# Optimization experiments

Measured on AMD Instinct MI355X. Metric: run time of the kernel, lower is better.

The kernel has to match this reference:

```python
import jax, jax.numpy as jnp
import numpy as np

D = 1024  # model_dim; d_ff == model_dim in this module
EPS = 1e-6

def setup_inputs() -> dict:
    key = jax.random.key(0)
    ks = jax.random.split(key, 8)
    s = 1.0 / np.sqrt(D)
    sg = 1.0 / np.sqrt(2 * D)
    return {
        "x": jax.random.normal(ks[0], (8, 2048, D), dtype=jnp.float32),
        "w1": jax.random.uniform(ks[1], (D, D), jnp.float32, -s, s),
        "b1": jnp.zeros((D,), jnp.float32),
        "w2": jax.random.uniform(ks[2], (D, D), jnp.float32, -s, s),
        "b2": jnp.zeros((D,), jnp.float32),
        "ln_g": jnp.ones((D,), jnp.float32),
        "ln_b": jnp.zeros((D,), jnp.float32),
        "wg": jax.random.uniform(ks[3], (2 * D, 2 * D), jnp.float32, -sg, sg),
        "bg": jnp.zeros((2 * D,), jnp.float32),
    }

def _layernorm(x, g, b):
    mu = jnp.mean(x, axis=-1, keepdims=True)
    var = jnp.mean(jnp.square(x - mu), axis=-1, keepdims=True)
    return (x - mu) * jax.lax.rsqrt(var + EPS) * g + b

def reference(x, w1, b1, w2, b2, ln_g, ln_b, wg, bg):
    B, S, d = x.shape
    # cumulative average: tril-normalized mask matmul == prefix-sum / position
    denom = jnp.arange(1, S + 1, dtype=x.dtype)[:, None]  # [S,1]
    avg = jnp.cumsum(x, axis=1) / denom                    # [B,S,D]
    # PositionwiseFeedForward (dropout is identity at inference)
    inter = jax.nn.relu(_layernorm(avg, ln_g, ln_b) @ w1 + b1)
    avg_out = inter @ w2 + b2 + avg
    # gating
    gates = jnp.concatenate([x, avg_out], axis=-1) @ wg + bg  # [B,S,2D]
    in_g, fg_g = jnp.split(gates, 2, axis=-1)
    gated = jax.nn.sigmoid(in_g) * x + jax.nn.sigmoid(fg_g) * avg_out
    return gated, avg_out
```

## Files before the change

### kernel.cpp

```cpp
#include <hip/hip_runtime.h>

typedef unsigned short u16;
typedef __attribute__((ext_vector_type(8))) short short8;
typedef __attribute__((ext_vector_type(8))) unsigned short ushort8;
typedef __attribute__((ext_vector_type(4))) float f32x4;
typedef __attribute__((ext_vector_type(4))) unsigned short u16x4;

#define DEV static __device__ __forceinline__

DEV u16 f2bf(float f){
    unsigned u = __float_as_uint(f);
    u += 0x7fffu + ((u >> 16) & 1u);
    return (u16)(u >> 16);
}
DEV float bf2f(u16 h){ return __uint_as_float(((unsigned)h) << 16); }
DEV float sigm(float v){ return 1.f / (1.f + __expf(-v)); }

DEV f32x4 MF(short8 a, short8 b, f32x4 c){
    return __builtin_amdgcn_mfma_f32_16x16x32_bf16(a, b, c, 0, 0, 0);
}
DEV void gload16(const void* g, u16* l){
    __builtin_amdgcn_global_load_lds(
        (const __attribute__((address_space(1))) void*)g,
        (__attribute__((address_space(3))) void*)l, 16, 0, 0);
}
DEV void stage_half(const char* gp, size_t K2, u16* dst){
    gload16(gp, dst);
    gload16(gp + (K2 << 3), dst + 512);
}

#define SBAR()   asm volatile("s_barrier" ::: "memory")
#define WVM(n)   asm volatile("s_waitcnt vmcnt(" #n ")" ::: "memory")
#define WLG0()   asm volatile("s_waitcnt lgkmcnt(0)" ::: "memory")

constexpr int Bn = 8, Sn = 2048, Dn = 1024;
constexpr int CH = 128, NC = Sn / CH;
constexpr size_t NTOK = (size_t)Bn * Sn;

__global__ __launch_bounds__(256) void k_wcvt(const float* __restrict__ w,
                                              u16* __restrict__ wt,
                                              int Kd, int Nd)
{
    __shared__ float tile[32][33];
    int nbn = Nd / 32;
    int bk = blockIdx.x / nbn, bn = blockIdx.x % nbn;
    int lx = threadIdx.x & 31, ly = threadIdx.x >> 5;
    #pragma unroll
    for (int i = 0; i < 32; i += 8)
        tile[ly + i][lx] = w[(size_t)(bk * 32 + ly + i) * Nd + bn * 32 + lx];
    __syncthreads();
    #pragma unroll
    for (int i = 0; i < 32; i += 8)
        wt[(size_t)(bn * 32 + ly + i) * Kd + bk * 32 + lx] = f2bf(tile[lx][ly + i]);
}

__global__ __launch_bounds__(256) void k_psum(const float* __restrict__ x,
                                              float* __restrict__ part)
{
    int bx = blockIdx.x;
    int dblk = bx & 3; bx >>= 2;
    int c = bx & (NC - 1), b = bx >> 4;
    int d = dblk * 256 + threadIdx.x;
    const float* px = x + ((size_t)b * Sn + (size_t)c * CH) * Dn + d;
    float s = 0.f;
    #pragma unroll 4
    for (int i = 0; i < CH; i++) s += px[(size_t)i * Dn];
    part[((size_t)b * NC + c) * Dn + d] = s;
}

__global__ __launch_bounds__(256) void k_pscan(float* part)
{
    int g = blockIdx.x * 256 + threadIdx.x;
    int b = g >> 10, d = g & 1023;
    float run = 0.f;
    #pragma unroll
    for (int c = 0; c < NC; c++){
        size_t idx = ((size_t)b * NC + c) * Dn + d;
        float v = part[idx]; part[idx] = run; run += v;
    }
}

__global__ __launch_bounds__(256) void k_avg(const float* __restrict__ x,
                                             const float* __restrict__ part,
                                             float* __restrict__ avg,
                                             u16* __restrict__ cat)
{
    int bx = blockIdx.x;
    int dblk = bx & 3; bx >>= 2;
    int c = bx & (NC - 1), b = bx >> 4;
    int d = dblk * 256 + threadIdx.x;
    const float* px = x   + ((size_t)b * Sn + (size_t)c * CH) * Dn + d;
    float*       pa = avg + ((size_t)b * Sn + (size_t)c * CH) * Dn + d;
    u16*         pc = cat + ((size_t)b * Sn + (size_t)c * CH) * 2048 + d;
    float run = part[((size_t)b * NC + c) * Dn + d];
    for (int i = 0; i < CH; i++){
        float v = px[(size_t)i * Dn];
        run += v;
        int s = c * CH + i;
        pa[(size_t)i * Dn] = run / (float)(s + 1);
        pc[(size_t)i * 2048] = f2bf(v);
    }
}

__global__ __launch_bounds__(256) void k_ln(const float* __restrict__ avg,
                                            const float* __restrict__ g,
                                            const float* __restrict__ bta,
                                            u16* __restrict__ out)
{
    size_t row = blockIdx.x;
    int t = threadIdx.x;
    const float4* pr = (const float4*)(avg + row * Dn);
    float4 v = pr[t];
    float s = v.x + v.y + v.z + v.w;
    float q = v.x * v.x + v.y * v.y + v.z * v.z + v.w * v.w;
    #pragma unroll
    for (int o = 32; o > 0; o >>= 1){
        s += __shfl_down(s, o, 64);
        q += __shfl_down(q, o, 64);
    }
    __shared__ float rs[4], rq[4];
    __shared__ float smu, srstd;
    int wid = t >> 6, lane = t & 63;
    if (lane == 0){ rs[wid] = s; rq[wid] = q; }
    __syncthreads();
    if (t == 0){
        float S = rs[0] + rs[1] + rs[2] + rs[3];
        float Q = rq[0] + rq[1] + rq[2] + rq[3];
        float mu = S * (1.f / Dn);
        float var = Q * (1.f / Dn) - mu * mu;
        smu = mu; srstd = rsqrtf(var + 1e-6f);
    }
    __syncthreads();
    float mu = smu, rstd = srstd;
    int d0 = t * 4;
    float4 gg = ((const float4*)g)[t];
    float4 bb = ((const float4*)bta)[t];
    u16x4 o;
    o[0] = f2bf((v.x - mu) * rstd * gg.x + bb.x);
    o[1] = f2bf((v.y - mu) * rstd * gg.y + bb.y);
    o[2] = f2bf((v.z - mu) * rstd * gg.z + bb.z);
    o[3] = f2bf((v.w - mu) * rstd * gg.w + bb.w);
    *(u16x4*)(out + row * Dn + d0) = o;
}

template<int EPI>
__global__ __launch_bounds__(512, 2)
void k_gemm(const u16* __restrict__ A, const u16* __restrict__ Bt,
            const float* __restrict__ bias,
            float* __restrict__ of, u16* __restrict__ ob,
            const float* __restrict__ resid,
            const float* __restrict__ xg, const float* __restrict__ ag,
            int M, int N, int K)
{
    __shared__ u16 smem[2][2][2][8192];

    int nbn = (EPI == 3) ? 8 : (N >> 8);
    int nwg = (M >> 8) * nbn;
    int bid = blockIdx.x;
    int swz = (bid & 7) * (nwg >> 3) + (bid >> 3);
    int bm = swz / nbn, bn = swz - bm * nbn;
    int m0 = bm << 8;
    int n0 = (EPI == 3) ? (bn << 7) : (bn << 8);

    int tid  = threadIdx.x;
    int wid  = tid >> 6, lane = tid & 63;
    int wm   = wid >> 2, wn = wid & 3;
    int fr   = lane & 15, q = lane >> 4;

    int srow = (wid << 4) + (lane >> 3);
    int cb   = ((lane & 7) << 4) ^ (((lane >> 3) & 7) << 4);
    size_t K2 = (size_t)K * 2;
    int b1base = (EPI == 3) ? (1024 + n0) : (n0 + 128);
    const char* gA0 = (const char*)A  + (size_t)(m0 + srow) * K2 + cb;
    const char* gA1 = (const char*)A  + (size_t)(m0 + 128 + srow) * K2 + cb;
    const char* gB0 = (const char*)Bt + (size_t)(n0 + srow) * K2 + cb;
    const char* gB1 = (const char*)Bt + (size_t)(b1base + srow) * K2 + cb;
    int w16 = wid << 10;

    int xorE = (lane & 7) << 3;
    int cbE0 = ((q << 3) ^ xorE);
    int cbE1 = cbE0 ^ 32;
    int aOff = (wm * 64 + fr) * 64;
    int bOff = (wn * 32 + fr) * 64;

    f32x4 acc[8][4] = {};
    int NT = K >> 6;

    stage_half(gA0, K2, &smem[0][0][0][w16]);
    stage_half(gB0, K2, &smem[0][1][0][w16]);
    stage_half(gB1, K2, &smem[0][1][1][w16]);
    stage_half(gA1, K2, &smem[0][0][1][w16]);

    for (int kt = 0; kt < NT; kt++){
        int cur = kt & 1, nxt = cur ^ 1;
        bool pre = (kt + 1) < NT;
        size_t toff = (size_t)(kt + 1) * 128;
        const u16* cA = &smem[cur][0][0][0];
        const u16* cB = &smem[cur][1][0][0];

        short8 a0f[4][2], a1f[4][2], b0f[2][2], b1f[2][2];

        WVM(4); SBAR();
        #pragma unroll
        for (int mi = 0; mi < 4; mi++){
            a0f[mi][0] = *(const short8*)&cA[aOff + mi * 1024 + cbE0];
            a0f[mi][1] = *(const short8*)&cA[aOff + mi * 1024 + cbE1];
        }
        #pragma unroll
        for (int ni = 0; ni < 2; ni++){
            b0f[ni][0] = *(const short8*)&cB[bOff + ni * 1024 + cbE0];
            b0f[ni][1] = *(const short8*)&cB[bOff + ni * 1024 + cbE1];
        }
        if (pre) stage_half(gA0 + toff, K2, &smem[nxt][0][0][w16]);
        WLG0();
        __builtin_amdgcn_sched_barrier(0);
        __builtin_amdgcn_s_setprio(1);
        #pragma unroll
        for (int mi = 0; mi < 4; mi++)
            #pragma unroll
            for (int ni = 0; ni < 2; ni++){
                acc[mi][ni] = MF(a0f[mi][0], b0f[ni][0], acc[mi][ni]);
                acc[mi][ni] = MF(a0f[mi][1], b0f[ni][1], acc[mi][ni]);
            }
        __builtin_amdgcn_s_setprio(0);

        if (pre){ WVM(4); } else { WVM(2); }
        SBAR();
        #pragma unroll
        for (int ni = 0; ni < 2; ni++){
            b1f[ni][0] = *(const short8*)&cB[8192 + bOff + ni * 1024 + cbE0];
            b1f[ni][1] = *(const short8*)&cB[8192 + bOff + ni * 1024 + cbE1];
        }
        if (pre) stage_half(gB0 + toff, K2, &smem[nxt][1][0][w16]);
        WLG0();
        __builtin_amdgcn_sched_barrier(0);
        __builtin_amdgcn_s_setprio(1);
        #pragma unroll
        for (int mi = 0; mi < 4; mi++)
            #pragma unroll
            for (int ni = 0; ni < 2; ni++){
                acc[mi][ni + 2] = MF(a0f[mi][0], b1f[ni][0], acc[mi][ni + 2]);
                acc[mi][ni + 2] = MF(a0f[mi][1], b1f[ni][1], acc[mi][ni + 2]);
            }
        __builtin_amdgcn_s_setprio(0);

        if (pre){ WVM(4); } else { WVM(0); }
        SBAR();
        #pragma unroll
        for (int mi = 0; mi < 4; mi++){
            a1f[mi][0] = *(const short8*)&cA[8192 + aOff + mi * 1024 + cbE0];
            a1f[mi][1] = *(const short8*)&cA[8192 + aOff + mi * 1024 + cbE1];
        }
        if (pre) stage_half(gB1 + toff, K2, &smem[nxt][1][1][w16]);
        WLG0();
        __builtin_amdgcn_sched_barrier(0);
        __builtin_amdgcn_s_setprio(1);
        #pragma unroll
        for (int mi = 0; mi < 4; mi++)
            #pragma unroll
            for (int ni = 0; ni < 2; ni++){
                acc[mi + 4][ni + 2] = MF(a1f[mi][0], b1f[ni][0], acc[mi + 4][ni + 2]);
                acc[mi + 4][ni + 2] = MF(a1f[mi][1], b1f[ni][1], acc[mi + 4][ni + 2]);
            }
        __builtin_amdgcn_s_setprio(0);

        if (pre) stage_half(gA1 + toff, K2, &smem[nxt][0][1][w16]);
        __builtin_amdgcn_s_setprio(1);
        #pragma unroll
        for (int mi = 0; mi < 4; mi++)
            #pragma unroll
            for (int ni = 0; ni < 2; ni++){
                acc[mi + 4][ni] = MF(a1f[mi][0], b0f[ni][0], acc[mi + 4][ni]);
                acc[mi + 4][ni] = MF(a1f[mi][1], b0f[ni][1], acc[mi + 4][ni]);
            }
        __builtin_amdgcn_s_setprio(0);
    }

    int col = lane & 15, rb = q * 4;

    if constexpr (EPI == 3){
        u16* s_in = &smem[0][0][0][0];
        u16* s_fg = s_in + 32768;
        float bi[2], bf_[2];
        #pragma unroll
        for (int ni = 0; ni < 2; ni++){
            bi[ni]  = bias[n0 + wn * 32 + ni * 16 + col];
            bf_[ni] = bias[1024 + n0 + wn * 32 + ni * 16 + col];
        }
        SBAR();
        #pragma unroll
        for (int mi = 0; mi < 8; mi++){
            int lrow = ((mi & 4) << 5) + wm * 64 + ((mi & 3) << 4) + rb;
            #pragma unroll
            for (int ni = 0; ni < 2; ni++){
                int c  = wn * 32 + ni * 16 + col;
                int cp = c ^ (q << 4);
                #pragma unroll
                for (int r = 0; r < 4; r++){
                    int row = lrow + r;
                    s_in[row * 128 + cp] = f2bf(sigm(acc[mi][ni][r] + bi[ni]));
                    s_fg[row * 128 + cp] = f2bf(sigm(acc[mi][ni + 2][r] + bf_[ni]));
                }
            }
        }
        WLG0(); SBAR();
        int rbase = wid * 32;
        #pragma unroll
        for (int rg = 0; rg < 8; rg++){
            int b4  = rbase + rg * 4;
            int row = b4 + (lane >> 4);
            int sw  = ((b4 >> 2) & 3) << 4;
            int c0  = (lane & 15) * 8;
            int cp  = c0 ^ sw;
            ushort8 iv = *(const ushort8*)&s_in[row * 128 + cp];
            ushort8 fv = *(const ushort8*)&s_fg[row * 128 + cp];
            size_t gb = (size_t)(m0 + row) * Dn + n0 + c0;
            float4 x0 = *(const float4*)&xg[gb], x1 = *(const float4*)&xg[gb + 4];
            float4 a0 = *(const float4*)&ag[gb], a1 = *(const float4*)&ag[gb + 4];
            float4 o0, o1;
            o0.x = bf2f(iv[0]) * x0.x + bf2f(fv[0]) * a0.x;
            o0.y = bf2f(iv[1]) * x0.y + bf2f(fv[1]) * a0.y;
            o0.z = bf2f(iv[2]) * x0.z + bf2f(fv[2]) * a0.z;
            o0.w = bf2f(iv[3]) * x0.w + bf2f(fv[3]) * a0.w;
            o1.x = bf2f(iv[4]) * x1.x + bf2f(fv[4]) * a1.x;
            o1.y = bf2f(iv[5]) * x1.y + bf2f(fv[5]) * a1.y;
            o1.z = bf2f(iv[6]) * x1.z + bf2f(fv[6]) * a1.z;
            o1.w = bf2f(iv[7]) * x1.w + bf2f(fv[7]) * a1.w;
            *(float4*)&of[gb] = o0;
            *(float4*)&of[gb + 4] = o1;
        }
        return;
    }

    #pragma unroll
    for (int mi = 0; mi < 8; mi++){
        int lrow = m0 + ((mi & 4) << 5) + wm * 64 + ((mi & 3) << 4) + rb;
        #pragma unroll
        for (int ni = 0; ni < 4; ni++){
            int gn = n0 + ((ni & 2) << 6) + wn * 32 + ((ni & 1) << 4) + col;
            float bv = bias[gn];
            #pragma unroll
            for (int r = 0; r < 4; r++){
                int gm = lrow + r;
                float v = acc[mi][ni][r] + bv;
                if constexpr (EPI == 1){
                    ob[(size_t)gm * N + gn] = f2bf(fmaxf(v, 0.f));
                } else {
                    v += resid[(size_t)gm * N + gn];
                    of[(size_t)gm * N + gn] = v;
                    ob[(size_t)gm * 2 * N + N + gn] = f2bf(v);
                }
            }
        }
    }
}

extern "C" void kernel_launch(void* const* d_in, const int* in_sizes, int n_in,
                              void* d_out, int out_size, void* d_ws, size_t ws_size,
                              hipStream_t stream)
{
    const float* x   = (const float*)d_in[0];
    const float* w1  = (const float*)d_in[1];
    const float* b1  = (const float*)d_in[2];
    const float* w2  = (const float*)d_in[3];
    const float* b2  = (const float*)d_in[4];
    const float* lng = (const float*)d_in[5];
    const float* lnb = (const float*)d_in[6];
    const float* wg  = (const float*)d_in[7];
    const float* bg  = (const float*)d_in[8];

    float* gated   = (float*)d_out;
    float* avg_out = (float*)d_out + NTOK * Dn;

    char* ws = (char*)d_ws;
    u16*   w1t   = (u16*)  (ws + (0ull   << 20));
    u16*   w2t   = (u16*)  (ws + (2ull   << 20));
    u16*   wgt   = (u16*)  (ws + (4ull   << 20));
    float* part  = (float*)(ws + (12ull  << 20));
    float* avg   = (float*)(ws + (16ull  << 20));
    u16*   ln    = (u16*)  (ws + (80ull  << 20));
    u16*   inter = (u16*)  (ws + (112ull << 20));
    u16*   cat   = (u16*)  (ws + (144ull << 20));

    k_wcvt<<<dim3(32 * 32), 256, 0, stream>>>(w1, w1t, Dn, Dn);
    k_wcvt<<<dim3(32 * 32), 256, 0, stream>>>(w2, w2t, Dn, Dn);
    k_wcvt<<<dim3(64 * 64), 256, 0, stream>>>(wg, wgt, 2 * Dn, 2 * Dn);

    k_psum <<<dim3(Bn * NC * 4), 256, 0, stream>>>(x, part);
    k_pscan<<<dim3(Bn * Dn / 256), 256, 0, stream>>>(part);
    k_avg  <<<dim3(Bn * NC * 4), 256, 0, stream>>>(x, part, avg, cat);

    k_ln<<<dim3((int)NTOK), 256, 0, stream>>>(avg, lng, lnb, ln);

    k_gemm<1><<<dim3((int)(NTOK / 256) * (Dn / 256)), 512, 0, stream>>>(
        ln, w1t, b1, nullptr, inter, nullptr, nullptr, nullptr,
        (int)NTOK, Dn, Dn);
    k_gemm<2><<<dim3((int)(NTOK / 256) * (Dn / 256)), 512, 0, stream>>>(
        inter, w2t, b2, avg_out, cat, avg, nullptr, nullptr,
        (int)NTOK, Dn, Dn);

    k_gemm<3><<<dim3((int)(NTOK / 256) * 8), 512, 0, stream>>>(
        cat, wgt, bg, gated, nullptr, nullptr, x, avg_out,
        (int)NTOK, 2 * Dn, 2 * Dn);
}
```

Measured before the change: 338.5 us.

## Store avg in bf16, reuse bf16 cat in gating epilogue, deepen GEMM prefetch pipeline

The cumulative average is now stored as bf16 instead of fp32, which halves its write and read traffic in the layernorm and GEMM2 residual steps. The gating epilogue reads bf16 x and avg_out from the cat buffer already in memory, replacing the fp32 reads of x and avg_out. The GEMM main loop is rewritten into a software pipeline that keeps two k-tiles in flight, with finer-grained vmcnt/lgkmcnt waits and sched barriers. This costs accuracy: avg enters the residual and layernorm in bf16, and gating multiplies by bf16-rounded x and avg_out.

```diff
diff --git a/kernel.cpp b/kernel.cpp
--- a/kernel.cpp
+++ b/kernel.cpp
@@ -31,7 +31,8 @@
 
 #define SBAR()   asm volatile("s_barrier" ::: "memory")
 #define WVM(n)   asm volatile("s_waitcnt vmcnt(" #n ")" ::: "memory")
-#define WLG0()   asm volatile("s_waitcnt lgkmcnt(0)" ::: "memory")
+#define WLG(n)   asm volatile("s_waitcnt lgkmcnt(" #n ")" ::: "memory")
+#define SCB()    __builtin_amdgcn_sched_barrier(0)
 
 constexpr int Bn = 8, Sn = 2048, Dn = 1024;
 constexpr int CH = 128, NC = Sn / CH;
@@ -82,7 +83,7 @@
 
 __global__ __launch_bounds__(256) void k_avg(const float* __restrict__ x,
                                              const float* __restrict__ part,
-                                             float* __restrict__ avg,
+                                             u16* __restrict__ avg,
                                              u16* __restrict__ cat)
 {
     int bx = blockIdx.x;
@@ -90,27 +91,27 @@
     int c = bx & (NC - 1), b = bx >> 4;
     int d = dblk * 256 + threadIdx.x;
     const float* px = x   + ((size_t)b * Sn + (size_t)c * CH) * Dn + d;
-    float*       pa = avg + ((size_t)b * Sn + (size_t)c * CH) * Dn + d;
+    u16*         pa = avg + ((size_t)b * Sn + (size_t)c * CH) * Dn + d;
     u16*         pc = cat + ((size_t)b * Sn + (size_t)c * CH) * 2048 + d;
     float run = part[((size_t)b * NC + c) * Dn + d];
     for (int i = 0; i < CH; i++){
         float v = px[(size_t)i * Dn];
         run += v;
         int s = c * CH + i;
-        pa[(size_t)i * Dn] = run / (float)(s + 1);
+        pa[(size_t)i * Dn] = f2bf(run / (float)(s + 1));
         pc[(size_t)i * 2048] = f2bf(v);
     }
 }
 
-__global__ __launch_bounds__(256) void k_ln(const float* __restrict__ avg,
+__global__ __launch_bounds__(256) void k_ln(const u16* __restrict__ avg,
                                             const float* __restrict__ g,
                                             const float* __restrict__ bta,
                                             u16* __restrict__ out)
 {
     size_t row = blockIdx.x;
     int t = threadIdx.x;
-    const float4* pr = (const float4*)(avg + row * Dn);
-    float4 v = pr[t];
+    u16x4 hv = ((const u16x4*)(avg + row * Dn))[t];
+    float4 v = { bf2f(hv[0]), bf2f(hv[1]), bf2f(hv[2]), bf2f(hv[3]) };
     float s = v.x + v.y + v.z + v.w;
     float q = v.x * v.x + v.y * v.y + v.z * v.z + v.w * v.w;
     #pragma unroll
@@ -148,8 +149,7 @@
 void k_gemm(const u16* __restrict__ A, const u16* __restrict__ Bt,
             const float* __restrict__ bias,
             float* __restrict__ of, u16* __restrict__ ob,
-            const float* __restrict__ resid,
-            const float* __restrict__ xg, const float* __restrict__ ag,
+            const u16* __restrict__ resid,
             int M, int N, int K)
 {
     __shared__ u16 smem[2][2][2][8192];
@@ -184,96 +184,91 @@
     int bOff = (wn * 32 + fr) * 64;
 
     f32x4 acc[8][4] = {};
+    short8 a0f[4][2], a1f[4][2], b0f[2][2], b1f[2][2];
     int NT = K >> 6;
 
-    stage_half(gA0, K2, &smem[0][0][0][w16]);
-    stage_half(gB0, K2, &smem[0][1][0][w16]);
-    stage_half(gB1, K2, &smem[0][1][1][w16]);
-    stage_half(gA1, K2, &smem[0][0][1][w16]);
-
-    for (int kt = 0; kt < NT; kt++){
-        int cur = kt & 1, nxt = cur ^ 1;
-        bool pre = (kt + 1) < NT;
-        size_t toff = (size_t)(kt + 1) * 128;
-        const u16* cA = &smem[cur][0][0][0];
-        const u16* cB = &smem[cur][1][0][0];
-
-        short8 a0f[4][2], a1f[4][2], b0f[2][2], b1f[2][2];
-
-        WVM(4); SBAR();
-        #pragma unroll
-        for (int mi = 0; mi < 4; mi++){
-            a0f[mi][0] = *(const short8*)&cA[aOff + mi * 1024 + cbE0];
-            a0f[mi][1] = *(const short8*)&cA[aOff + mi * 1024 + cbE1];
-        }
-        #pragma unroll
-        for (int ni = 0; ni < 2; ni++){
-            b0f[ni][0] = *(const short8*)&cB[bOff + ni * 1024 + cbE0];
-            b0f[ni][1] = *(const short8*)&cB[bOff + ni * 1024 + cbE1];
-        }
-        if (pre) stage_half(gA0 + toff, K2, &smem[nxt][0][0][w16]);
-        WLG0();
-        __builtin_amdgcn_sched_barrier(0);
-        __builtin_amdgcn_s_setprio(1);
-        #pragma unroll
-        for (int mi = 0; mi < 4; mi++)
-            #pragma unroll
-            for (int ni = 0; ni < 2; ni++){
-                acc[mi][ni] = MF(a0f[mi][0], b0f[ni][0], acc[mi][ni]);
-                acc[mi][ni] = MF(a0f[mi][1], b0f[ni][1], acc[mi][ni]);
-            }
-        __builtin_amdgcn_s_setprio(0);
-
-        if (pre){ WVM(4); } else { WVM(2); }
+#define ST_A0(t) stage_half(gA0 + (size_t)(t) * 128, K2, &smem[(t)&1][0][0][w16])
+#define ST_A1(t) stage_half(gA1 + (size_t)(t) * 128, K2, &smem[(t)&1][0][1][w16])
+#define ST_B0(t) stage_half(gB0 + (size_t)(t) * 128, K2, &smem[(t)&1][1][0][w16])
+#define ST_B1(t) stage_half(gB1 + (size_t)(t) * 128, K2, &smem[(t)&1][1][1][w16])
+#define RD_A(Fr, t, half) { const u16* _p = &smem[(t)&1][0][half][0];           \
+    _Pragma("unroll") for (int i = 0; i < 4; i++){                              \
+        Fr[i][0] = *(const short8*)&_p[aOff + i * 1024 + cbE0];                 \
+        Fr[i][1] = *(const short8*)&_p[aOff + i * 1024 + cbE1]; } }
+#define RD_B(Fr, t, half) { const u16* _p = &smem[(t)&1][1][half][0];           \
+    _Pragma("unroll") for (int i = 0; i < 2; i++){                              \
+        Fr[i][0] = *(const short8*)&_p[bOff + i * 1024 + cbE0];                 \
+        Fr[i][1] = *(const short8*)&_p[bOff + i * 1024 + cbE1]; } }
+#define MMQ(Af, Bf, mo, no)                                                     \
+    __builtin_amdgcn_s_setprio(1);                                              \
+    _Pragma("unroll") for (int mi = 0; mi < 4; mi++)                            \
+        _Pragma("unroll") for (int ni = 0; ni < 2; ni++){                       \
+            acc[mi+(mo)][ni+(no)] = MF(Af[mi][0], Bf[ni][0], acc[mi+(mo)][ni+(no)]); \
+            acc[mi+(mo)][ni+(no)] = MF(Af[mi][1], Bf[ni][1], acc[mi+(mo)][ni+(no)]); \
+        }                                                                        \
+    __builtin_amdgcn_s_setprio(0);
+
+    ST_A0(0); ST_B0(0); ST_B1(0); ST_A1(0); ST_A0(1); ST_B0(1); ST_B1(1);
+    WVM(12); SBAR();
+    RD_A(a0f, 0, 0);
+
+    for (int t = 0; t + 2 < NT; ++t){
+        WVM(8); SBAR();
+        ST_A1(t + 1);
+        RD_B(b0f, t, 0); SCB();
+        RD_B(b1f, t, 1);
+        WLG(4); SCB();
+        MMQ(a0f, b0f, 0, 0);
+        WVM(8); SBAR();
+        ST_A0(t + 2);
+        RD_A(a1f, t, 1);
+        WLG(8); SCB();
+        MMQ(a0f, b1f, 0, 2);
         SBAR();
-        #pragma unroll
-        for (int ni = 0; ni < 2; ni++){
-            b1f[ni][0] = *(const short8*)&cB[8192 + bOff + ni * 1024 + cbE0];
-            b1f[ni][1] = *(const short8*)&cB[8192 + bOff + ni * 1024 + cbE1];
-        }
-        if (pre) stage_half(gB0 + toff, K2, &smem[nxt][1][0][w16]);
-        WLG0();
-        __builtin_amdgcn_sched_barrier(0);
-        __builtin_amdgcn_s_setprio(1);
-        #pragma unroll
-        for (int mi = 0; mi < 4; mi++)
-            #pragma unroll
-            for (int ni = 0; ni < 2; ni++){
-                acc[mi][ni + 2] = MF(a0f[mi][0], b1f[ni][0], acc[mi][ni + 2]);
-                acc[mi][ni + 2] = MF(a0f[mi][1], b1f[ni][1], acc[mi][ni + 2]);
-            }
-        __builtin_amdgcn_s_setprio(0);
-
-        if (pre){ WVM(4); } else { WVM(0); }
+        ST_B0(t + 2);
+        WLG(0); SCB();
+        MMQ(a1f, b1f, 4, 2);
+        WVM(10); SBAR();
+        ST_B1(t + 2);
+        RD_A(a0f, t + 1, 0);
+        WLG(8); SCB();
+        MMQ(a1f, b0f, 4, 0);
+    }
+    {
+        int t = NT - 2;
+        WVM(8); SBAR();
+        ST_A1(t + 1);
+        RD_B(b0f, t, 0); SCB();
+        RD_B(b1f, t, 1);
+        WLG(4); SCB();
+        MMQ(a0f, b0f, 0, 0);
+        WVM(8); SBAR();
+        RD_A(a1f, t, 1);
+        WLG(8); SCB();
+        MMQ(a0f, b1f, 0, 2);
         SBAR();
-        #pragma unroll
-        for (int mi = 0; mi < 4; mi++){
-            a1f[mi][0] = *(const short8*)&cA[8192 + aOff + mi * 1024 + cbE0];
-            a1f[mi][1] = *(const short8*)&cA[8192 + aOff + mi * 1024 + cbE1];
-        }
-        if (pre) stage_half(gB1 + toff, K2, &smem[nxt][1][1][w16]);
-        WLG0();
-        __builtin_amdgcn_sched_barrier(0);
-        __builtin_amdgcn_s_setprio(1);
-        #pragma unroll
-        for (int mi = 0; mi < 4; mi++)
-            #pragma unroll
-            for (int ni = 0; ni < 2; ni++){
-                acc[mi + 4][ni + 2] = MF(a1f[mi][0], b1f[ni][0], acc[mi + 4][ni + 2]);
-                acc[mi + 4][ni + 2] = MF(a1f[mi][1], b1f[ni][1], acc[mi + 4][ni + 2]);
-            }
-        __builtin_amdgcn_s_setprio(0);
-
-        if (pre) stage_half(gA1 + toff, K2, &smem[nxt][0][1][w16]);
-        __builtin_amdgcn_s_setprio(1);
-        #pragma unroll
-        for (int mi = 0; mi < 4; mi++)
-            #pragma unroll
-            for (int ni = 0; ni < 2; ni++){
-                acc[mi + 4][ni] = MF(a1f[mi][0], b0f[ni][0], acc[mi + 4][ni]);
-                acc[mi + 4][ni] = MF(a1f[mi][1], b0f[ni][1], acc[mi + 4][ni]);
-            }
-        __builtin_amdgcn_s_setprio(0);
+        WLG(0); SCB();
+        MMQ(a1f, b1f, 4, 2);
+        WVM(6); SBAR();
+        RD_A(a0f, t + 1, 0);
+        WLG(8); SCB();
+        MMQ(a1f, b0f, 4, 0);
+    }
+    {
+        int t = NT - 1;
+        WVM(2); SBAR();
+        RD_B(b0f, t, 0); SCB();
+        RD_B(b1f, t, 1);
+        WLG(4); SCB();
+        MMQ(a0f, b0f, 0, 0);
+        WVM(0); SBAR();
+        RD_A(a1f, t, 1);
+        WLG(8); SCB();
+        MMQ(a0f, b1f, 0, 2);
+        SBAR();
+        WLG(0); SCB();
+        MMQ(a1f, b1f, 4, 2);
+        MMQ(a1f, b0f, 4, 0);
     }
 
     int col = lane & 15, rb = q * 4;
@@ -303,7 +298,7 @@
                 }
             }
         }
-        WLG0(); SBAR();
+        WLG(0); SBAR();
         int rbase = wid * 32;
         #pragma unroll
         for (int rg = 0; rg < 8; rg++){
@@ -314,18 +309,19 @@
             int cp  = c0 ^ sw;
             ushort8 iv = *(const ushort8*)&s_in[row * 128 + cp];
             ushort8 fv = *(const ushort8*)&s_fg[row * 128 + cp];
+            size_t ga = (size_t)(m0 + row) * 2048 + n0 + c0;
+            ushort8 xv = *(const ushort8*)&A[ga];
+            ushort8 av = *(const ushort8*)&A[ga + 1024];
             size_t gb = (size_t)(m0 + row) * Dn + n0 + c0;
-            float4 x0 = *(const float4*)&xg[gb], x1 = *(const float4*)&xg[gb + 4];
-            float4 a0 = *(const float4*)&ag[gb], a1 = *(const float4*)&ag[gb + 4];
             float4 o0, o1;
-            o0.x = bf2f(iv[0]) * x0.x + bf2f(fv[0]) * a0.x;
-            o0.y = bf2f(iv[1]) * x0.y + bf2f(fv[1]) * a0.y;
-            o0.z = bf2f(iv[2]) * x0.z + bf2f(fv[2]) * a0.z;
-            o0.w = bf2f(iv[3]) * x0.w + bf2f(fv[3]) * a0.w;
-            o1.x = bf2f(iv[4]) * x1.x + bf2f(fv[4]) * a1.x;
-            o1.y = bf2f(iv[5]) * x1.y + bf2f(fv[5]) * a1.y;
-            o1.z = bf2f(iv[6]) * x1.z + bf2f(fv[6]) * a1.z;
-            o1.w = bf2f(iv[7]) * x1.w + bf2f(fv[7]) * a1.w;
+            o0.x = bf2f(iv[0]) * bf2f(xv[0]) + bf2f(fv[0]) * bf2f(av[0]);
+            o0.y = bf2f(iv[1]) * bf2f(xv[1]) + bf2f(fv[1]) * bf2f(av[1]);
+            o0.z = bf2f(iv[2]) * bf2f(xv[2]) + bf2f(fv[2]) * bf2f(av[2]);
+            o0.w = bf2f(iv[3]) * bf2f(xv[3]) + bf2f(fv[3]) * bf2f(av[3]);
+            o1.x = bf2f(iv[4]) * bf2f(xv[4]) + bf2f(fv[4]) * bf2f(av[4]);
+            o1.y = bf2f(iv[5]) * bf2f(xv[5]) + bf2f(fv[5]) * bf2f(av[5]);
+            o1.z = bf2f(iv[6]) * bf2f(xv[6]) + bf2f(fv[6]) * bf2f(av[6]);
+            o1.w = bf2f(iv[7]) * bf2f(xv[7]) + bf2f(fv[7]) * bf2f(av[7]);
             *(float4*)&of[gb] = o0;
             *(float4*)&of[gb + 4] = o1;
         }
@@ -346,7 +342,7 @@
                 if constexpr (EPI == 1){
                     ob[(size_t)gm * N + gn] = f2bf(fmaxf(v, 0.f));
                 } else {
-                    v += resid[(size_t)gm * N + gn];
+                    v += bf2f(resid[(size_t)gm * N + gn]);
                     of[(size_t)gm * N + gn] = v;
                     ob[(size_t)gm * 2 * N + N + gn] = f2bf(v);
                 }
@@ -377,7 +373,7 @@
     u16*   w2t   = (u16*)  (ws + (2ull   << 20));
     u16*   wgt   = (u16*)  (ws + (4ull   << 20));
     float* part  = (float*)(ws + (12ull  << 20));
-    float* avg   = (float*)(ws + (16ull  << 20));
+    u16*   avg   = (u16*)  (ws + (16ull  << 20));
     u16*   ln    = (u16*)  (ws + (80ull  << 20));
     u16*   inter = (u16*)  (ws + (112ull << 20));
     u16*   cat   = (u16*)  (ws + (144ull << 20));
@@ -393,13 +389,10 @@
     k_ln<<<dim3((int)NTOK), 256, 0, stream>>>(avg, lng, lnb, ln);
 
     k_gemm<1><<<dim3((int)(NTOK / 256) * (Dn / 256)), 512, 0, stream>>>(
-        ln, w1t, b1, nullptr, inter, nullptr, nullptr, nullptr,
-        (int)NTOK, Dn, Dn);
+        ln, w1t, b1, nullptr, inter, nullptr, (int)NTOK, Dn, Dn);
     k_gemm<2><<<dim3((int)(NTOK / 256) * (Dn / 256)), 512, 0, stream>>>(
-        inter, w2t, b2, avg_out, cat, avg, nullptr, nullptr,
-        (int)NTOK, Dn, Dn);
+        inter, w2t, b2, avg_out, cat, avg, (int)NTOK, Dn, Dn);
 
     k_gemm<3><<<dim3((int)(NTOK / 256) * 8), 512, 0, stream>>>(
-        cat, wgt, bg, gated, nullptr, nullptr, x, avg_out,
-        (int)NTOK, 2 * Dn, 2 * Dn);
-}
+        cat, wgt, bg, gated, nullptr, nullptr, (int)NTOK, 2 * Dn, 2 * Dn);
+}
```

Result: faster. 302.3 us (-10.7%).
